# Kernel tuning notes

Measured on AMD Instinct MI355X. Metric: run time of the kernel, lower is better.

The kernel has to match this reference:

```python
import jax, jax.numpy as jnp
import numpy as np

N = 100000        # nodes
E = 1600000       # edges
NFEAT = 500
NHID = [256, 128]
NCLASS = 40
K = 10
ALPHA = 0.1


def setup_inputs() -> dict:
    key = jax.random.key(0)
    ks = jax.random.split(key, 9)
    x = jax.random.normal(ks[0], (N, NFEAT), dtype=jnp.float32)
    edge_index = jax.random.randint(ks[1], (2, E), 0, N, dtype=jnp.int32)
    dims = [NFEAT] + NHID + [NCLASS]
    # Linear params (PyTorch convention: W is [out, in])
    W0 = jax.random.normal(ks[2], (dims[1], dims[0]), jnp.float32) / np.sqrt(dims[0])
    b0 = jnp.zeros((dims[1],), jnp.float32)
    W1 = jax.random.normal(ks[3], (dims[2], dims[1]), jnp.float32) / np.sqrt(dims[1])
    b1 = jnp.zeros((dims[2],), jnp.float32)
    W2 = jax.random.normal(ks[4], (dims[3], dims[2]), jnp.float32) / np.sqrt(dims[2])
    b2 = jnp.zeros((dims[3],), jnp.float32)
    return {"x": x, "edge_index": edge_index,
            "W0": W0, "b0": b0, "W1": W1, "b1": b1, "W2": W2, "b2": b2}


def reference(x, edge_index, W0, b0, W1, b1, W2, b2):
    # MLP encoder: ReLU after every Linear (dropout is identity in eval mode)
    h = x
    for W, b in ((W0, b0), (W1, b1), (W2, b2)):
        h = jax.nn.relu(h @ W.T + b)   # [N, out]

    # --- APPNP propagation with GCN normalization (self-loops added) ---
    loops = jnp.arange(N, dtype=edge_index.dtype)
    src = jnp.concatenate([edge_index[0], loops])  # [E+N]
    dst = jnp.concatenate([edge_index[1], loops])  # [E+N]
    deg = jnp.zeros((N,), h.dtype).at[dst].add(jnp.ones_like(dst, h.dtype))
    dinv = jax.lax.rsqrt(deg)                      # deg >= 1 due to self-loops
    norm = dinv[src] * dinv[dst]                   # [E+N]

    h0 = h
    for _ in range(K):
        msg = h[src] * norm[:, None]               # gather + scale, [E+N, C]
        agg = jnp.zeros_like(h).at[dst].add(msg)   # scatter-add, [N, C]
        h = (1.0 - ALPHA) * agg + ALPHA * h0       # teleport fusion
    return h
```

## Files before the change

kernel.cpp:

```cpp
#include <hip/hip_runtime.h>

#define NN 100000
#define EE 1600000
#define KITER 10

typedef __attribute__((ext_vector_type(8))) short s16x8;
typedef __attribute__((ext_vector_type(4))) float f32x4;

__device__ __forceinline__ short f2bf(float f) {
    union { float f; unsigned u; } v; v.f = f;
    unsigned r = v.u + 0x7FFFu + ((v.u >> 16) & 1u);
    return (short)(r >> 16);
}

__device__ __forceinline__ void gload_lds16(const void* g, void* l) {
    __builtin_amdgcn_global_load_lds(
        (const __attribute__((address_space(1))) void*)g,
        (__attribute__((address_space(3))) void*)l, 16, 0, 0);
}

template<int KSTEPS, bool OUT_BF16>
__global__ __launch_bounds__(256)
void mfma_gemm(const short* __restrict__ A, int lda, const short* __restrict__ B,
               const float* __restrict__ bias, int nbias,
               void* __restrict__ Cout, int ldc, int ncols_store, int nrows)
{
    __shared__ short ldsA[128 * 32];
    __shared__ short ldsB[128 * 32];
    const int t    = threadIdx.x;
    const int lane = t & 63;
    const int wid  = t >> 6;
    const int rowBase = blockIdx.y * 128;
    const int colBase = blockIdx.x * 128;
    const int wrow = (wid >> 1) * 64;
    const int wcol = (wid & 1) * 64;

    const int q  = t & 3;
    const int rl = t >> 2;

    f32x4 acc[4][4] = {};
    const int KPB = KSTEPS * 32;

    for (int ks = 0; ks < KSTEPS; ++ks) {
        const int k0 = ks * 32;

        #pragma unroll
        for (int i = 0; i < 2; ++i) {
            const short* srcB = B + (size_t)(colBase + rl + i * 64) * KPB + k0 + q * 8;
            gload_lds16(srcB, &ldsB[wid * 512 + i * 2048]);
        }
        #pragma unroll
        for (int i = 0; i < 2; ++i) {
            int grow = rowBase + rl + i * 64; if (grow > NN - 1) grow = NN - 1;
            const short* srcA = A + (size_t)grow * lda + k0 + q * 8;
            gload_lds16(srcA, &ldsA[wid * 512 + i * 2048]);
        }

        __syncthreads();

        {
            const int kb = lane >> 4;
            const int l16 = lane & 15;
            s16x8 a[4], b[4];
            #pragma unroll
            for (int m = 0; m < 4; ++m)
                a[m] = *(const s16x8*)&ldsA[(wrow + m * 16 + l16) * 32 + kb * 8];
            #pragma unroll
            for (int n = 0; n < 4; ++n)
                b[n] = *(const s16x8*)&ldsB[(wcol + n * 16 + l16) * 32 + kb * 8];
            #pragma unroll
            for (int m = 0; m < 4; ++m)
                #pragma unroll
                for (int n = 0; n < 4; ++n)
                    acc[m][n] = __builtin_amdgcn_mfma_f32_16x16x32_bf16(
                        a[m], b[n], acc[m][n], 0, 0, 0);
        }

        __syncthreads();
    }

    const int crow0 = (lane >> 4) * 4;
    const int ccol  = lane & 15;
    #pragma unroll
    for (int n = 0; n < 4; ++n) {
        int col = colBase + wcol + n * 16 + ccol;
        float bv = (col < nbias) ? bias[col] : 0.f;
        #pragma unroll
        for (int m = 0; m < 4; ++m) {
            #pragma unroll
            for (int j = 0; j < 4; ++j) {
                int row = rowBase + wrow + m * 16 + crow0 + j;
                if (row >= nrows) continue;
                float v = acc[m][n][j] + bv;
                v = fmaxf(v, 0.f);
                if (OUT_BF16) {
                    ((short*)Cout)[(size_t)row * ldc + col] = f2bf(v);
                } else if (col < ncols_store) {
                    ((float*)Cout)[(size_t)row * ldc + col] = v;
                }
            }
        }
    }
}

__global__ void convert_x_kernel(const float* __restrict__ in, short* __restrict__ out) {
    int idx = blockIdx.x * blockDim.x + threadIdx.x;
    if (idx >= (NN * 500) / 8) return;
    const float4* in4 = (const float4*)in;
    float4 a = in4[(size_t)idx * 2];
    float4 b = in4[(size_t)idx * 2 + 1];
    s16x8 s;
    s[0]=f2bf(a.x); s[1]=f2bf(a.y); s[2]=f2bf(a.z); s[3]=f2bf(a.w);
    s[4]=f2bf(b.x); s[5]=f2bf(b.y); s[6]=f2bf(b.z); s[7]=f2bf(b.w);
    *(s16x8*)&out[(size_t)idx * 8] = s;
}

__global__ void convert_w_kernel(const float* __restrict__ in, short* __restrict__ out,
                                 int R, int C, int Rp, int Cp) {
    int idx = blockIdx.x * blockDim.x + threadIdx.x;
    if (idx >= Rp * Cp) return;
    int r = idx / Cp, c = idx - r * Cp;
    float v = (r < R && c < C) ? in[r * C + c] : 0.f;
    out[idx] = f2bf(v);
}

__global__ void deg_init_kernel(int* deg, int n) {
    int i = blockIdx.x * blockDim.x + threadIdx.x;
    if (i < n) deg[i] = 1;
}
__global__ void deg_count_kernel(const int* __restrict__ dst, int* deg, int e) {
    int i = blockIdx.x * blockDim.x + threadIdx.x;
    if (i < e) atomicAdd(&deg[dst[i]], 1);
}
__global__ void dinv_kernel(const int* __restrict__ deg, float* __restrict__ dinv,
                            float* __restrict__ dinv2, int n) {
    int i = blockIdx.x * blockDim.x + threadIdx.x;
    if (i < n) {
        float d = (float)deg[i];
        dinv[i] = rsqrtf(d);
        dinv2[i] = 1.0f / d;
    }
}
__global__ __launch_bounds__(256)
void scan1_kernel(const int* __restrict__ deg, int* __restrict__ row_ptr,
                  int* __restrict__ blockSums, int n) {
    __shared__ int sdata[256];
    const int base = blockIdx.x * 2048;
    const int t = threadIdx.x;
    int local[8];
    int s = 0;
    #pragma unroll
    for (int i = 0; i < 8; ++i) {
        int idx = base + t * 8 + i;
        int c = (idx < n) ? (deg[idx] - 1) : 0;
        local[i] = s;
        s += c;
    }
    sdata[t] = s;
    __syncthreads();
    for (int off = 1; off < 256; off <<= 1) {
        int v = (t >= off) ? sdata[t - off] : 0;
        __syncthreads();
        sdata[t] += v;
        __syncthreads();
    }
    int excl = (t == 0) ? 0 : sdata[t - 1];
    #pragma unroll
    for (int i = 0; i < 8; ++i) {
        int idx = base + t * 8 + i;
        if (idx < n) row_ptr[idx] = excl + local[i];
    }
    if (t == 255) blockSums[blockIdx.x] = sdata[255];
}
__global__ void scan2_kernel(int* blockSums, int nb) {
    if (threadIdx.x == 0 && blockIdx.x == 0) {
        int s = 0;
        for (int i = 0; i < nb; ++i) { int v = blockSums[i]; blockSums[i] = s; s += v; }
    }
}
__global__ void scan3_kernel(int* __restrict__ row_ptr, int* __restrict__ cursor,
                             const int* __restrict__ blockSums, int n, int e) {
    int i = blockIdx.x * blockDim.x + threadIdx.x;
    if (i < n) {
        int v = row_ptr[i] + blockSums[i >> 11];
        row_ptr[i] = v;
        cursor[i] = v;
    }
    if (i == 0) row_ptr[n] = e;
}
__global__ void fill_csr_kernel(const int* __restrict__ src, const int* __restrict__ dst,
                                const float* __restrict__ dinv, int* cursor,
                                int2* __restrict__ pairs, int e) {
    int i = blockIdx.x * blockDim.x + threadIdx.x;
    if (i < e) {
        int s = src[i], d = dst[i];
        int pos = atomicAdd(&cursor[d], 1);
        float nv = dinv[s] * dinv[d];
        pairs[pos] = make_int2(s, __float_as_int(nv));
    }
}

__global__ __launch_bounds__(320)
void prop_kernel(const float4* __restrict__ hin4, const float4* __restrict__ h04,
                 const int* __restrict__ rowp, const int2* __restrict__ pairs,
                 const float* __restrict__ dinv2, float4* __restrict__ hout4, int n)
{
    const int t = threadIdx.x;
    const int vl = t / 10;
    const int f4 = t - vl * 10;
    const int v = blockIdx.x * 32 + vl;
    if (v >= n) return;
    const size_t base = (size_t)v * 10 + f4;

    float4 sf = hin4[base];
    const float dv = dinv2[v];
    float ax = dv * sf.x, ay = dv * sf.y, az = dv * sf.z, aw = dv * sf.w;

    int e = rowp[v];
    const int e1 = rowp[v + 1];

    for (; e + 4 <= e1; e += 4) {
        int2 p0 = pairs[e], p1 = pairs[e + 1], p2 = pairs[e + 2], p3 = pairs[e + 3];
        float4 g0 = hin4[(size_t)p0.x * 10 + f4];
        float4 g1 = hin4[(size_t)p1.x * 10 + f4];
        float4 g2 = hin4[(size_t)p2.x * 10 + f4];
        float4 g3 = hin4[(size_t)p3.x * 10 + f4];
        float w0 = __int_as_float(p0.y), w1 = __int_as_float(p1.y);
        float w2 = __int_as_float(p2.y), w3 = __int_as_float(p3.y);
        ax = fmaf(w0, g0.x, ax); ay = fmaf(w0, g0.y, ay);
        az = fmaf(w0, g0.z, az); aw = fmaf(w0, g0.w, aw);
        ax = fmaf(w1, g1.x, ax); ay = fmaf(w1, g1.y, ay);
        az = fmaf(w1, g1.z, az); aw = fmaf(w1, g1.w, aw);
        ax = fmaf(w2, g2.x, ax); ay = fmaf(w2, g2.y, ay);
        az = fmaf(w2, g2.z, az); aw = fmaf(w2, g2.w, aw);
        ax = fmaf(w3, g3.x, ax); ay = fmaf(w3, g3.y, ay);
        az = fmaf(w3, g3.z, az); aw = fmaf(w3, g3.w, aw);
    }
    for (; e < e1; ++e) {
        int2 p = pairs[e];
        float4 g = hin4[(size_t)p.x * 10 + f4];
        float w = __int_as_float(p.y);
        ax = fmaf(w, g.x, ax); ay = fmaf(w, g.y, ay);
        az = fmaf(w, g.z, az); aw = fmaf(w, g.w, aw);
    }

    float4 h0v = h04[base];
    float4 o;
    o.x = fmaf(0.9f, ax, 0.1f * h0v.x);
    o.y = fmaf(0.9f, ay, 0.1f * h0v.y);
    o.z = fmaf(0.9f, az, 0.1f * h0v.z);
    o.w = fmaf(0.9f, aw, 0.1f * h0v.w);
    hout4[base] = o;
}

extern "C" void kernel_launch(void* const* d_in, const int* in_sizes, int n_in,
                              void* d_out, int out_size, void* d_ws, size_t ws_size,
                              hipStream_t stream) {
    const float* x  = (const float*)d_in[0];
    const int* ei   = (const int*)d_in[1];
    const float* W0 = (const float*)d_in[2];
    const float* b0 = (const float*)d_in[3];
    const float* W1 = (const float*)d_in[4];
    const float* b1 = (const float*)d_in[5];
    const float* W2 = (const float*)d_in[6];
    const float* b2 = (const float*)d_in[7];
    float* out = (float*)d_out;
    char* ws = (char*)d_ws;

    const int* src = ei;
    const int* dst = ei + EE;

    short* xb   = (short*)(ws);
    short* h1b  = (short*)(ws + 100000000);
    short* W0b  = (short*)(ws + 151200000);
    short* W1b  = (short*)(ws + 151462144);
    short* W2b  = (short*)(ws + 151527680);

    short* h2b  = (short*)(ws);
    float* h0   = (float*)(ws + 25600000);
    float* hA   = (float*)(ws + 41600000);
    float* hB   = (float*)(ws + 57600000);

    int2*  pairs= (int2*) (ws + 100000000);
    int*   deg  = (int*)  (ws + 112800000);
    float* dinv = (float*)(ws + 113200000);
    float* dnv2 = (float*)(ws + 113600000);
    int*   rowp = (int*)  (ws + 114000000);
    int*   curs = (int*)  (ws + 114400008);
    int*   bsum = (int*)  (ws + 114800008);
    (void)ws_size; (void)in_sizes; (void)n_in; (void)out_size;

    convert_x_kernel<<<((NN * 500 / 8) + 255) / 256, 256, 0, stream>>>(x, xb);
    convert_w_kernel<<<(256 * 512 + 255) / 256, 256, 0, stream>>>(W0, W0b, 256, 500, 256, 512);
    convert_w_kernel<<<(128 * 256 + 255) / 256, 256, 0, stream>>>(W1, W1b, 128, 256, 128, 256);
    convert_w_kernel<<<(128 * 128 + 255) / 256, 256, 0, stream>>>(W2, W2b, 40, 128, 128, 128);

    const int NBLK = (NN + 127) / 128;
    mfma_gemm<16, true ><<<dim3(2, NBLK), 256, 0, stream>>>(
        xb, 500, W0b, b0, 256, (void*)h1b, 256, 256, NN);
    mfma_gemm<8,  true ><<<dim3(1, NBLK), 256, 0, stream>>>(
        h1b, 256, W1b, b1, 128, (void*)h2b, 128, 128, NN);
    mfma_gemm<4,  false><<<dim3(1, NBLK), 256, 0, stream>>>(
        h2b, 128, W2b, b2, 40, (void*)h0, 40, 40, NN);

    {
        int nb_n = (NN + 255) / 256;
        int nb_e = (EE + 255) / 256;
        deg_init_kernel<<<nb_n, 256, 0, stream>>>(deg, NN);
        deg_count_kernel<<<nb_e, 256, 0, stream>>>(dst, deg, EE);
        dinv_kernel<<<nb_n, 256, 0, stream>>>(deg, dinv, dnv2, NN);
        int nb_scan = (NN + 2047) / 2048;
        scan1_kernel<<<nb_scan, 256, 0, stream>>>(deg, rowp, bsum, NN);
        scan2_kernel<<<1, 64, 0, stream>>>(bsum, nb_scan);
        scan3_kernel<<<nb_n, 256, 0, stream>>>(rowp, curs, bsum, NN, EE);
        fill_csr_kernel<<<nb_e, 256, 0, stream>>>(src, dst, dinv, curs, pairs, EE);
    }

    {
        dim3 blk(320);
        dim3 grd((NN + 31) / 32);
        const float* hin = h0;
        for (int it = 0; it < KITER; ++it) {
            float* hout = (it == KITER - 1) ? out : ((it & 1) ? hB : hA);
            prop_kernel<<<grd, blk, 0, stream>>>(
                (const float4*)hin, (const float4*)h0, rowp, pairs, dnv2,
                (float4*)hout, NN);
            hin = hout;
        }
    }
}
```

Baseline: 895.6 us.

## Store propagation features in 8-wide planes and gather per plane

The final GEMM now writes h0 in a planar layout: five planes of 8 features, each plane contiguous across all nodes. The propagation kernel gives each thread one destination node and one 8-feature plane, and block indices are interleaved so that different planes of the same destination range run together. Gathers then touch a compact 8 MB plane instead of the full 16 MB feature matrix, which is meant to improve L2 locality. The cost is that each block re-reads the CSR pairs once per plane, and the final iteration scatters its result back into row-major output.

```diff
diff --git a/kernel.cpp b/kernel.cpp
--- a/kernel.cpp
+++ b/kernel.cpp
@@ -19,7 +19,7 @@
         (__attribute__((address_space(3))) void*)l, 16, 0, 0);
 }
 
-template<int KSTEPS, bool OUT_BF16>
+template<int KSTEPS, bool OUT_BF16, bool PLANAR>
 __global__ __launch_bounds__(256)
 void mfma_gemm(const short* __restrict__ A, int lda, const short* __restrict__ B,
                const float* __restrict__ bias, int nbias,
@@ -96,7 +96,10 @@
                 if (OUT_BF16) {
                     ((short*)Cout)[(size_t)row * ldc + col] = f2bf(v);
                 } else if (col < ncols_store) {
-                    ((float*)Cout)[(size_t)row * ldc + col] = v;
+                    if (PLANAR)
+                        ((float*)Cout)[((size_t)(col >> 3) * NN + row) * 8 + (col & 7)] = v;
+                    else
+                        ((float*)Cout)[(size_t)row * ldc + col] = v;
                 }
             }
         }
@@ -200,57 +203,93 @@
     }
 }
 
-__global__ __launch_bounds__(320)
-void prop_kernel(const float4* __restrict__ hin4, const float4* __restrict__ h04,
-                 const int* __restrict__ rowp, const int2* __restrict__ pairs,
-                 const float* __restrict__ dinv2, float4* __restrict__ hout4, int n)
+#define NB_DST 391
+__global__ __launch_bounds__(256)
+void prop_plane_kernel(const float4* __restrict__ hinP, const float4* __restrict__ h0P,
+                       const int* __restrict__ rowp, const int2* __restrict__ pairs,
+                       const float* __restrict__ dinv2, float4* __restrict__ houtP,
+                       float* __restrict__ outFinal)
 {
-    const int t = threadIdx.x;
-    const int vl = t / 10;
-    const int f4 = t - vl * 10;
-    const int v = blockIdx.x * 32 + vl;
-    if (v >= n) return;
-    const size_t base = (size_t)v * 10 + f4;
-
-    float4 sf = hin4[base];
-    const float dv = dinv2[v];
-    float ax = dv * sf.x, ay = dv * sf.y, az = dv * sf.z, aw = dv * sf.w;
-
-    int e = rowp[v];
-    const int e1 = rowp[v + 1];
+    const int s = blockIdx.x & 7;
+    const int j = blockIdx.x >> 3;
+    int plane, dstblk;
+    if (s < 3)      { if (j >= 196) return; plane = s;     dstblk = 2 * j; }
+    else if (s < 5) {                       plane = s;     dstblk = j; }
+    else            { if (j >= 195) return; plane = s - 5; dstblk = 2 * j + 1; }
+    const int dst = dstblk * 256 + threadIdx.x;
+    if (dst >= NN) return;
+
+    const float4* hp = hinP + (size_t)plane * NN * 2;
+    const size_t self = (size_t)dst * 2;
+
+    float4 a0, a1;
+    {
+        const float dv = dinv2[dst];
+        float4 s0 = hp[self], s1 = hp[self + 1];
+        a0.x = dv * s0.x; a0.y = dv * s0.y; a0.z = dv * s0.z; a0.w = dv * s0.w;
+        a1.x = dv * s1.x; a1.y = dv * s1.y; a1.z = dv * s1.z; a1.w = dv * s1.w;
+    }
+
+    int e = rowp[dst];
+    const int e1 = rowp[dst + 1];
 
     for (; e + 4 <= e1; e += 4) {
         int2 p0 = pairs[e], p1 = pairs[e + 1], p2 = pairs[e + 2], p3 = pairs[e + 3];
-        float4 g0 = hin4[(size_t)p0.x * 10 + f4];
-        float4 g1 = hin4[(size_t)p1.x * 10 + f4];
-        float4 g2 = hin4[(size_t)p2.x * 10 + f4];
-        float4 g3 = hin4[(size_t)p3.x * 10 + f4];
+        const size_t i0 = (size_t)p0.x * 2, i1 = (size_t)p1.x * 2;
+        const size_t i2 = (size_t)p2.x * 2, i3 = (size_t)p3.x * 2;
+        float4 g00 = hp[i0], g01 = hp[i0 + 1];
+        float4 g10 = hp[i1], g11 = hp[i1 + 1];
+        float4 g20 = hp[i2], g21 = hp[i2 + 1];
+        float4 g30 = hp[i3], g31 = hp[i3 + 1];
         float w0 = __int_as_float(p0.y), w1 = __int_as_float(p1.y);
         float w2 = __int_as_float(p2.y), w3 = __int_as_float(p3.y);
-        ax = fmaf(w0, g0.x, ax); ay = fmaf(w0, g0.y, ay);
-        az = fmaf(w0, g0.z, az); aw = fmaf(w0, g0.w, aw);
-        ax = fmaf(w1, g1.x, ax); ay = fmaf(w1, g1.y, ay);
-        az = fmaf(w1, g1.z, az); aw = fmaf(w1, g1.w, aw);
-        ax = fmaf(w2, g2.x, ax); ay = fmaf(w2, g2.y, ay);
-        az = fmaf(w2, g2.z, az); aw = fmaf(w2, g2.w, aw);
-        ax = fmaf(w3, g3.x, ax); ay = fmaf(w3, g3.y, ay);
-        az = fmaf(w3, g3.z, az); aw = fmaf(w3, g3.w, aw);
+        a0.x = fmaf(w0, g00.x, a0.x); a0.y = fmaf(w0, g00.y, a0.y);
+        a0.z = fmaf(w0, g00.z, a0.z); a0.w = fmaf(w0, g00.w, a0.w);
+        a1.x = fmaf(w0, g01.x, a1.x); a1.y = fmaf(w0, g01.y, a1.y);
+        a1.z = fmaf(w0, g01.z, a1.z); a1.w = fmaf(w0, g01.w, a1.w);
+        a0.x = fmaf(w1, g10.x, a0.x); a0.y = fmaf(w1, g10.y, a0.y);
+        a0.z = fmaf(w1, g10.z, a0.z); a0.w = fmaf(w1, g10.w, a0.w);
+        a1.x = fmaf(w1, g11.x, a1.x); a1.y = fmaf(w1, g11.y, a1.y);
+        a1.z = fmaf(w1, g11.z, a1.z); a1.w = fmaf(w1, g11.w, a1.w);
+        a0.x = fmaf(w2, g20.x, a0.x); a0.y = fmaf(w2, g20.y, a0.y);
+        a0.z = fmaf(w2, g20.z, a0.z); a0.w = fmaf(w2, g20.w, a0.w);
+        a1.x = fmaf(w2, g21.x, a1.x); a1.y = fmaf(w2, g21.y, a1.y);
+        a1.z = fmaf(w2, g21.z, a1.z); a1.w = fmaf(w2, g21.w, a1.w);
+        a0.x = fmaf(w3, g30.x, a0.x); a0.y = fmaf(w3, g30.y, a0.y);
+        a0.z = fmaf(w3, g30.z, a0.z); a0.w = fmaf(w3, g30.w, a0.w);
+        a1.x = fmaf(w3, g31.x, a1.x); a1.y = fmaf(w3, g31.y, a1.y);
+        a1.z = fmaf(w3, g31.z, a1.z); a1.w = fmaf(w3, g31.w, a1.w);
     }
     for (; e < e1; ++e) {
         int2 p = pairs[e];
-        float4 g = hin4[(size_t)p.x * 10 + f4];
+        const size_t i0 = (size_t)p.x * 2;
+        float4 g0 = hp[i0], g1 = hp[i0 + 1];
         float w = __int_as_float(p.y);
-        ax = fmaf(w, g.x, ax); ay = fmaf(w, g.y, ay);
-        az = fmaf(w, g.z, az); aw = fmaf(w, g.w, aw);
-    }
-
-    float4 h0v = h04[base];
-    float4 o;
-    o.x = fmaf(0.9f, ax, 0.1f * h0v.x);
-    o.y = fmaf(0.9f, ay, 0.1f * h0v.y);
-    o.z = fmaf(0.9f, az, 0.1f * h0v.z);
-    o.w = fmaf(0.9f, aw, 0.1f * h0v.w);
-    hout4[base] = o;
+        a0.x = fmaf(w, g0.x, a0.x); a0.y = fmaf(w, g0.y, a0.y);
+        a0.z = fmaf(w, g0.z, a0.z); a0.w = fmaf(w, g0.w, a0.w);
+        a1.x = fmaf(w, g1.x, a1.x); a1.y = fmaf(w, g1.y, a1.y);
+        a1.z = fmaf(w, g1.z, a1.z); a1.w = fmaf(w, g1.w, a1.w);
+    }
+
+    const float4* h0p = h0P + (size_t)plane * NN * 2;
+    float4 h00 = h0p[self], h01 = h0p[self + 1];
+    float4 o0, o1;
+    o0.x = fmaf(0.9f, a0.x, 0.1f * h00.x);
+    o0.y = fmaf(0.9f, a0.y, 0.1f * h00.y);
+    o0.z = fmaf(0.9f, a0.z, 0.1f * h00.z);
+    o0.w = fmaf(0.9f, a0.w, 0.1f * h00.w);
+    o1.x = fmaf(0.9f, a1.x, 0.1f * h01.x);
+    o1.y = fmaf(0.9f, a1.y, 0.1f * h01.y);
+    o1.z = fmaf(0.9f, a1.z, 0.1f * h01.z);
+    o1.w = fmaf(0.9f, a1.w, 0.1f * h01.w);
+
+    if (outFinal) {
+        float4* op = (float4*)(outFinal + (size_t)dst * 40 + plane * 8);
+        op[0] = o0; op[1] = o1;
+    } else {
+        float4* op = houtP + (size_t)plane * NN * 2 + self;
+        op[0] = o0; op[1] = o1;
+    }
 }
 
 extern "C" void kernel_launch(void* const* d_in, const int* in_sizes, int n_in,
@@ -296,11 +335,11 @@
     convert_w_kernel<<<(128 * 128 + 255) / 256, 256, 0, stream>>>(W2, W2b, 40, 128, 128, 128);
 
     const int NBLK = (NN + 127) / 128;
-    mfma_gemm<16, true ><<<dim3(2, NBLK), 256, 0, stream>>>(
+    mfma_gemm<16, true,  false><<<dim3(2, NBLK), 256, 0, stream>>>(
         xb, 500, W0b, b0, 256, (void*)h1b, 256, 256, NN);
-    mfma_gemm<8,  true ><<<dim3(1, NBLK), 256, 0, stream>>>(
+    mfma_gemm<8,  true,  false><<<dim3(1, NBLK), 256, 0, stream>>>(
         h1b, 256, W1b, b1, 128, (void*)h2b, 128, 128, NN);
-    mfma_gemm<4,  false><<<dim3(1, NBLK), 256, 0, stream>>>(
+    mfma_gemm<4,  false, true ><<<dim3(1, NBLK), 256, 0, stream>>>(
         h2b, 128, W2b, b2, 40, (void*)h0, 40, 40, NN);
 
     {
@@ -317,15 +356,16 @@
     }
 
     {
-        dim3 blk(320);
-        dim3 grd((NN + 31) / 32);
+        dim3 blk(256);
+        dim3 grd(8 * NB_DST);
         const float* hin = h0;
         for (int it = 0; it < KITER; ++it) {
-            float* hout = (it == KITER - 1) ? out : ((it & 1) ? hB : hA);
-            prop_kernel<<<grd, blk, 0, stream>>>(
+            float* houtP = (it & 1) ? hB : hA;
+            float* fin   = (it == KITER - 1) ? out : nullptr;
+            prop_plane_kernel<<<grd, blk, 0, stream>>>(
                 (const float4*)hin, (const float4*)h0, rowp, pairs, dnv2,
-                (float4*)hout, NN);
-            hin = hout;
-        }
-    }
-}
+                (float4*)houtP, fin);
+            hin = houtP;
+        }
+    }
+}
```

New measurement: 1.592 ms. 77.7% more time.
